# Kernel tuning notes

Hardware: AMD Instinct MI355X
Metric: run time of the kernel (lower is better)

Reference implementation:

```python
import jax, jax.numpy as jnp
import numpy as np

B, S, D_MODEL, FILTER, K, MAX_FRAMES = 16, 512, 512, 512, 3, 2048


def _conv1d(x, w, b):
    # x: [B, C, L], w: [O, I, K], padding=1 -> same length
    y = jax.lax.conv_general_dilated(x, w, window_strides=(1,), padding=[(1, 1)],
                                     dimension_numbers=("NCH", "OIH", "NCH"))
    return y + b[None, :, None]


def _predictor(x, w1, b1, w2, b2, wl, bl):
    # x: [B, L, d] -> scalar track [B, L]
    h = x.transpose(0, 2, 1)                      # [B, d, L]
    h = jax.nn.relu(_conv1d(h, w1, b1))
    h = jax.nn.relu(_conv1d(h, w2, b2))
    h = h.transpose(0, 2, 1)                      # [B, L, filter]
    return (jnp.einsum("blf,f->bl", h, wl[:, 0]) + bl[0])


def _expand_hidden(H, D, max_T):
    # Length regulator: cumsum + searchsorted gather (vectorized repeat_interleave).
    D = jnp.maximum(D, 0).astype(jnp.int32)
    csum = jnp.cumsum(D, axis=1)                  # [B, S]
    t = jnp.arange(max_T, dtype=jnp.int32)        # [T]
    # idx[b, t] = # of cumsum entries <= t  == source token index for frame t
    idx = jax.vmap(lambda c: jnp.searchsorted(c, t, side="right"))(csum)  # [B, T]
    total = csum[:, -1]                           # [B]
    valid = t[None, :] < jnp.minimum(total, max_T)[:, None]               # [B, T]
    idx_safe = jnp.minimum(idx, S - 1)
    He = jnp.take_along_axis(H, idx_safe[:, :, None], axis=1)             # [B, T, d]
    return jnp.where(valid[:, :, None], He, jnp.zeros((), He.dtype))


def setup_inputs() -> dict:
    key = jax.random.key(0)
    ks = jax.random.split(key, 24)
    def w(k, shape, scale=0.05):
        return jax.random.normal(k, shape, dtype=jnp.float32) * scale
    inp = {
        "H": jax.random.normal(ks[0], (B, S, D_MODEL), dtype=jnp.float32),
        "D_gt": jax.random.randint(ks[1], (B, S), 0, 12, dtype=jnp.int32),
        "P_gt": jax.random.normal(ks[2], (B, MAX_FRAMES), dtype=jnp.float32),
        "E_gt": jax.random.normal(ks[3], (B, MAX_FRAMES), dtype=jnp.float32),
    }
    for i, p in enumerate(["dp", "pp", "ep"]):
        kk = jax.random.split(ks[4 + i], 3)
        inp[p + "_w1"] = w(kk[0], (FILTER, D_MODEL, K))
        inp[p + "_b1"] = jnp.zeros((FILTER,), jnp.float32)
        inp[p + "_w2"] = w(kk[1], (FILTER, FILTER, K))
        inp[p + "_b2"] = jnp.zeros((FILTER,), jnp.float32)
        inp[p + "_wl"] = w(kk[2], (FILTER, 1))
        inp[p + "_bl"] = jnp.zeros((1,), jnp.float32)
    inp["pitch_w"] = w(ks[8], (D_MODEL,))
    inp["pitch_b"] = jnp.zeros((D_MODEL,), jnp.float32)
    inp["energy_w"] = w(ks[9], (D_MODEL,))
    inp["energy_b"] = jnp.zeros((D_MODEL,), jnp.float32)
    return inp


def reference(H, D_gt, P_gt, E_gt,
              dp_w1, dp_b1, dp_w2, dp_b2, dp_wl, dp_bl,
              pp_w1, pp_b1, pp_w2, pp_b2, pp_wl, pp_bl,
              ep_w1, ep_b1, ep_w2, ep_b2, ep_wl, ep_bl,
              pitch_w, pitch_b, energy_w, energy_b):
    # Training path (is_inference=False): D = D_gt, P = P_gt, E = E_gt.
    D_pred = _predictor(H, dp_w1, dp_b1, dp_w2, dp_b2, dp_wl, dp_bl)     # [B, S]
    H_exp = _expand_hidden(H, D_gt, MAX_FRAMES)                           # [B, T, d]
    P_pred = _predictor(H_exp, pp_w1, pp_b1, pp_w2, pp_b2, pp_wl, pp_bl)  # [B, T]
    E_pred = _predictor(H_exp, ep_w1, ep_b1, ep_w2, ep_b2, ep_wl, ep_bl)  # [B, T]
    P_proj = P_gt[:, :, None] * pitch_w[None, None, :] + pitch_b          # Linear(1,d)
    E_proj = E_gt[:, :, None] * energy_w[None, None, :] + energy_b
    H_adapted = H_exp + P_proj + E_proj
    return (H_adapted, D_pred, P_pred, E_pred)
```

## Files before the change

kernel.cpp:

```cpp
#include <hip/hip_runtime.h>

#define B_ 16
#define S_ 512
#define C_ 512
#define T_ 2048

typedef __attribute__((ext_vector_type(8))) short short8;
typedef __attribute__((ext_vector_type(4))) float floatx4;

__device__ __forceinline__ unsigned short f2bf(float x) {
    union { float f; unsigned u; } c; c.f = x;
    unsigned r = (c.u + 0x7fffu + ((c.u >> 16) & 1u)) >> 16;
    return (unsigned short)r;
}

__device__ __forceinline__ void gld_lds16(void* l, const void* g) {
    __builtin_amdgcn_global_load_lds(
        (const __attribute__((address_space(1))) void*)g,
        (__attribute__((address_space(3))) void*)l, 16, 0, 0);
}

__global__ void prep_kernel(const float* __restrict__ w0, const float* __restrict__ w1,
                            const float* __restrict__ w2, const float* __restrict__ w3,
                            const float* __restrict__ w4, const float* __restrict__ w5,
                            unsigned short* __restrict__ wpack,
                            const float* __restrict__ H, unsigned short* __restrict__ Hbf,
                            unsigned short* __restrict__ zrow) {
    int blk = blockIdx.x;
    if (blk < 6144) {
        int which = blk >> 10;
        const float* w = which == 0 ? w0 : which == 1 ? w1 : which == 2 ? w2
                       : which == 3 ? w3 : which == 4 ? w4 : w5;
        unsigned short* wp = wpack + (long)which * 786432;
        int i = (blk & 1023) * 256 + threadIdx.x;
        const float* s = w + (long)i * 3;
        wp[i]          = f2bf(s[0]);
        wp[i + 262144] = f2bf(s[1]);
        wp[i + 524288] = f2bf(s[2]);
    } else if (blk < 10240) {
        int i = (blk - 6144) * 256 + threadIdx.x;
        float4 v = *(const float4*)(H + (long)i * 4);
        ushort4 o;
        o.x = f2bf(v.x); o.y = f2bf(v.y); o.z = f2bf(v.z); o.w = f2bf(v.w);
        *(ushort4*)(Hbf + (long)i * 4) = o;
    } else {
        zrow[(blk - 10240) * 256 + threadIdx.x] = 0;
    }
}

__global__ void expand_rowidx_kernel(const int* __restrict__ Dgt, int* __restrict__ ridx) {
    __shared__ int cs[S_];
    int b = blockIdx.x, s = threadIdx.x;
    int d = Dgt[b * S_ + s];
    cs[s] = d < 0 ? 0 : d;
    __syncthreads();
    for (int off = 1; off < S_; off <<= 1) {
        int v = (s >= off) ? cs[s - off] : 0;
        __syncthreads();
        cs[s] += v;
        __syncthreads();
    }
    int total = cs[S_ - 1];
    int limit = total < T_ ? total : T_;
    for (int t = s; t < T_; t += S_) {
        int lo = 0, hi = S_;
        while (lo < hi) { int mid = (lo + hi) >> 1; if (cs[mid] <= t) lo = mid + 1; else hi = mid; }
        if (lo > S_ - 1) lo = S_ - 1;
        ridx[b * T_ + t] = (t < limit) ? lo : -1;
    }
}

__global__ void fill3_kernel(float* __restrict__ D, float* __restrict__ P, float* __restrict__ E,
                             const float* __restrict__ dbl, const float* __restrict__ pbl,
                             const float* __restrict__ ebl) {
    int i = blockIdx.x * 256 + threadIdx.x;
    if (i < 8192) D[i] = dbl[0];
    else if (i < 40960) P[i - 8192] = pbl[0];
    else E[i - 40960] = ebl[0];
}

__global__ void adapt_kernel(const float* __restrict__ H, const int* __restrict__ ridx,
                             const float* __restrict__ Pgt, const float* __restrict__ Egt,
                             const float* __restrict__ pw, const float* __restrict__ pb,
                             const float* __restrict__ ew, const float* __restrict__ eb,
                             float* __restrict__ out) {
    int i = blockIdx.x * 256 + threadIdx.x;
    int f4 = i & 127;
    int p  = i >> 7;
    int b  = p >> 11;
    int r  = ridx[p];
    float pg = Pgt[p], eg = Egt[p];
    int f = f4 << 2;
    float4 pwv = *(const float4*)(pw + f);
    float4 pbv = *(const float4*)(pb + f);
    float4 ewv = *(const float4*)(ew + f);
    float4 ebv = *(const float4*)(eb + f);
    float4 h = make_float4(0.f, 0.f, 0.f, 0.f);
    if (r >= 0) h = *(const float4*)(H + ((long)b * S_ + r) * C_ + f);
    float4 o;
    o.x = h.x + pg * pwv.x + pbv.x + eg * ewv.x + ebv.x;
    o.y = h.y + pg * pwv.y + pbv.y + eg * ewv.y + ebv.y;
    o.z = h.z + pg * pwv.z + pbv.z + eg * ewv.z + ebv.z;
    o.w = h.w + pg * pwv.w + pbv.w + eg * ewv.w + ebv.w;
    *(float4*)(out + (long)p * C_ + f) = o;
}

struct ConvJob {
    const unsigned short* X;
    const int* ridx;
    int Lshift;
    int Bshift;
    const unsigned short* wp;
    const float* bias;
    const float* wl;
    void* dst;
    int nx;
};

__global__ __launch_bounds__(256, 4) void conv_mfma_kernel(
    ConvJob j0, ConvJob j1, const unsigned short* __restrict__ zrow, int mode)
{
    __shared__ unsigned short Wt[3 * 128 * 32];
    __shared__ unsigned short Xt[136 * 32];
    const ConvJob j = (blockIdx.y < 4) ? j0 : j1;
    if ((int)blockIdx.x >= j.nx) return;
    const int tid = threadIdx.x;
    const int m0 = (blockIdx.y & 3) * 128;
    const int n0 = blockIdx.x * 128;
    const int L = 1 << j.Lshift;
    const int b = n0 >> j.Lshift;
    const int t0 = n0 & (L - 1);

    floatx4 acc[4][4];
#pragma unroll
    for (int i = 0; i < 4; ++i)
#pragma unroll
        for (int jj = 0; jj < 4; ++jj) acc[i][jj] = (floatx4){0.f, 0.f, 0.f, 0.f};

    const unsigned short* wptr[6];
#pragma unroll
    for (int q = 0; q < 6; ++q) {
        int idx = tid + q * 256;
        int tap = idx >> 9, rem = idx & 511;
        int row = rem >> 2;
        int sw = (rem & 3) ^ ((row >> 1) & 3);
        wptr[q] = j.wp + (long)tap * (C_ * C_) + (long)(m0 + row) * C_ + sw * 8;
    }
    auto xrow = [&](int rho) -> const unsigned short* {
        int t = t0 - 1 + rho;
        if (t < 0 || t >= L) return zrow;
        int r = j.ridx ? j.ridx[(b << j.Lshift) + t] : t;
        if (r < 0) return zrow;
        return j.X + ((long)(b << j.Bshift) + r) * C_;
    };
    const int xs = tid & 3;
    const int rho0 = tid >> 2, rho1 = 64 + (tid >> 2), rho2 = 128 + (tid >> 2);
    const unsigned short* xptr0 = xrow(rho0) + (xs ^ ((rho0 >> 1) & 3)) * 8;
    const unsigned short* xptr1 = xrow(rho1) + (xs ^ ((rho1 >> 1) & 3)) * 8;
    const unsigned short* xptr2 = (tid < 8) ? (xrow(rho2) + (xs ^ ((rho2 >> 1) & 3)) * 8) : zrow;

    char* wbase = (char*)Wt + (tid >> 6) * 1024;
    char* xbase = (char*)Xt + (tid >> 6) * 1024;

    const int lane = tid & 63;
    const int q = lane >> 4, lr = lane & 15;
    const int wm = (tid >> 6) & 1, wn = tid >> 7;
    const int qsW = (q ^ ((lr >> 1) & 3)) * 8;
    int qsX[3];
#pragma unroll
    for (int tap = 0; tap < 3; ++tap)
        qsX[tap] = (q ^ (((lr + tap) >> 1) & 3)) * 8;

    for (int c0 = 0; c0 < C_; c0 += 32) {
        __syncthreads();
#pragma unroll
        for (int qq = 0; qq < 6; ++qq)
            gld_lds16(wbase + qq * 4096, wptr[qq] + c0);
        gld_lds16(xbase, xptr0 + c0);
        gld_lds16(xbase + 4096, xptr1 + c0);
        if (tid < 8)
            gld_lds16((char*)Xt + 8192, xptr2 + c0);
        __syncthreads();
#pragma unroll
        for (int tap = 0; tap < 3; ++tap) {
            const unsigned short* Wl = Wt + ((tap * 128) + wm * 64 + lr) * 32 + qsW;
            const unsigned short* Xl = Xt + (wn * 64 + lr + tap) * 32 + qsX[tap];
            short8 a[4], bf[4];
#pragma unroll
            for (int i = 0; i < 4; ++i) {
                a[i]  = *(const short8*)(Wl + i * 16 * 32);
                bf[i] = *(const short8*)(Xl + i * 16 * 32);
            }
#pragma unroll
            for (int i = 0; i < 4; ++i)
#pragma unroll
                for (int jj = 0; jj < 4; ++jj)
                    acc[i][jj] = __builtin_amdgcn_mfma_f32_16x16x32_bf16(
                        a[i], bf[jj], acc[i][jj], 0, 0, 0);
        }
    }

    const int fbase = m0 + wm * 64 + q * 4;
    const int pbase = n0 + wn * 64 + lr;
    if (mode == 0) {
        unsigned short* dst = (unsigned short*)j.dst;
#pragma unroll
        for (int i = 0; i < 4; ++i) {
            int f = fbase + i * 16;
            float4 bv = *(const float4*)(j.bias + f);
#pragma unroll
            for (int jj = 0; jj < 4; ++jj) {
                int p = pbase + jj * 16;
                ushort4 o;
                o.x = f2bf(fmaxf(acc[i][jj][0] + bv.x, 0.f));
                o.y = f2bf(fmaxf(acc[i][jj][1] + bv.y, 0.f));
                o.z = f2bf(fmaxf(acc[i][jj][2] + bv.z, 0.f));
                o.w = f2bf(fmaxf(acc[i][jj][3] + bv.w, 0.f));
                *(ushort4*)(dst + (long)p * C_ + f) = o;
            }
        }
    } else {
        float* dst = (float*)j.dst;
#pragma unroll
        for (int jj = 0; jj < 4; ++jj) {
            float s = 0.f;
#pragma unroll
            for (int i = 0; i < 4; ++i) {
                int f = fbase + i * 16;
                float4 bv = *(const float4*)(j.bias + f);
                float4 wv = *(const float4*)(j.wl + f);
                s += fmaxf(acc[i][jj][0] + bv.x, 0.f) * wv.x;
                s += fmaxf(acc[i][jj][1] + bv.y, 0.f) * wv.y;
                s += fmaxf(acc[i][jj][2] + bv.z, 0.f) * wv.z;
                s += fmaxf(acc[i][jj][3] + bv.w, 0.f) * wv.w;
            }
            s += __shfl_xor(s, 16, 64);
            s += __shfl_xor(s, 32, 64);
            if (lane < 16) atomicAdd(dst + pbase + jj * 16, s);
        }
    }
}

extern "C" void kernel_launch(void* const* d_in, const int* in_sizes, int n_in,
                              void* d_out, int out_size, void* d_ws, size_t ws_size,
                              hipStream_t stream) {
    const float* H    = (const float*)d_in[0];
    const int*   Dgt  = (const int*)d_in[1];
    const float* Pgt  = (const float*)d_in[2];
    const float* Egt  = (const float*)d_in[3];
    const float* dp_w1 = (const float*)d_in[4];
    const float* dp_b1 = (const float*)d_in[5];
    const float* dp_w2 = (const float*)d_in[6];
    const float* dp_b2 = (const float*)d_in[7];
    const float* dp_wl = (const float*)d_in[8];
    const float* dp_bl = (const float*)d_in[9];
    const float* pp_w1 = (const float*)d_in[10];
    const float* pp_b1 = (const float*)d_in[11];
    const float* pp_w2 = (const float*)d_in[12];
    const float* pp_b2 = (const float*)d_in[13];
    const float* pp_wl = (const float*)d_in[14];
    const float* pp_bl = (const float*)d_in[15];
    const float* ep_w1 = (const float*)d_in[16];
    const float* ep_b1 = (const float*)d_in[17];
    const float* ep_w2 = (const float*)d_in[18];
    const float* ep_b2 = (const float*)d_in[19];
    const float* ep_wl = (const float*)d_in[20];
    const float* ep_bl = (const float*)d_in[21];
    const float* pitch_w  = (const float*)d_in[22];
    const float* pitch_b  = (const float*)d_in[23];
    const float* energy_w = (const float*)d_in[24];
    const float* energy_b = (const float*)d_in[25];

    float* out     = (float*)d_out;
    float* H_adapt = out;
    float* D_pred  = out + 16777216;
    float* P_pred  = out + 16785408;
    float* E_pred  = out + 16818176;

    char* ws = (char*)d_ws;
    size_t off = 0;
    unsigned short* wpack = (unsigned short*)(ws + off); off += 6UL * 786432UL * 2UL;
    unsigned short* Hbf   = (unsigned short*)(ws + off); off += 4194304UL * 2UL;
    unsigned short* h1a   = (unsigned short*)(ws + off); off += 16777216UL * 2UL;
    unsigned short* h1dp  = (unsigned short*)(ws + off); off += 4194304UL * 2UL;
    unsigned short* zrow  = (unsigned short*)(ws + off); off += 512UL * 2UL;
    off = (off + 255) & ~(size_t)255;
    int* ridx_exp = (int*)(ws + off); off += (size_t)B_ * T_ * 4;

    hipLaunchKernelGGL(prep_kernel, dim3(10242), dim3(256), 0, stream,
                       dp_w1, dp_w2, pp_w1, pp_w2, ep_w1, ep_w2, wpack, H, Hbf, zrow);
    hipLaunchKernelGGL(expand_rowidx_kernel, dim3(B_), dim3(S_), 0, stream, Dgt, ridx_exp);
    hipLaunchKernelGGL(adapt_kernel, dim3(16384), dim3(256), 0, stream,
                       H, ridx_exp, Pgt, Egt, pitch_w, pitch_b, energy_w, energy_b, H_adapt);
    hipLaunchKernelGGL(fill3_kernel, dim3(288), dim3(256), 0, stream,
                       D_pred, P_pred, E_pred, dp_bl, pp_bl, ep_bl);

    ConvJob j_pp1 = { Hbf, ridx_exp, 11, 9, wpack + 2UL * 786432, pp_b1, nullptr, h1a,  256 };
    ConvJob j_dp1 = { Hbf, nullptr,   9, 9, wpack + 0UL * 786432, dp_b1, nullptr, h1dp,  64 };
    ConvJob j_pp2 = { h1a, nullptr,  11, 11, wpack + 3UL * 786432, pp_b2, pp_wl, P_pred, 256 };
    ConvJob j_dp2 = { h1dp, nullptr,  9,  9, wpack + 1UL * 786432, dp_b2, dp_wl, D_pred,  64 };
    ConvJob j_ep1 = { Hbf, ridx_exp, 11, 9, wpack + 4UL * 786432, ep_b1, nullptr, h1a,  256 };
    ConvJob j_ep2 = { h1a, nullptr,  11, 11, wpack + 5UL * 786432, ep_b2, ep_wl, E_pred, 256 };

    hipLaunchKernelGGL(conv_mfma_kernel, dim3(256, 8), dim3(256), 0, stream, j_pp1, j_dp1, zrow, 0);
    hipLaunchKernelGGL(conv_mfma_kernel, dim3(256, 8), dim3(256), 0, stream, j_pp2, j_dp2, zrow, 1);
    hipLaunchKernelGGL(conv_mfma_kernel, dim3(256, 4), dim3(256), 0, stream, j_ep1, j_ep1, zrow, 0);
    hipLaunchKernelGGL(conv_mfma_kernel, dim3(256, 4), dim3(256), 0, stream, j_ep2, j_ep2, zrow, 1);
}
```

Before: 387.9 us.

## Fuse prep kernels and co-schedule pitch/energy/duration convs with adapt in mega kernel

Folds the row-index scan and bias fill into the prep kernel, and merges the adapt gather into the first conv launch as extra blocks. With a second hidden buffer, the pitch, energy and duration conv layers run together in two launches instead of four. The goal is fewer launches, less tail idling and better overlap of the bandwidth-bound adapt pass with MFMA conv work. The cost is an extra 32MB workspace buffer; the new path is gated on the workspace size, with a fallback otherwise.

```diff
diff --git a/kernel.cpp b/kernel.cpp
--- a/kernel.cpp
+++ b/kernel.cpp
@@ -25,84 +25,64 @@
                             const float* __restrict__ w4, const float* __restrict__ w5,
                             unsigned short* __restrict__ wpack,
                             const float* __restrict__ H, unsigned short* __restrict__ Hbf,
-                            unsigned short* __restrict__ zrow) {
+                            unsigned short* __restrict__ zrow,
+                            const int* __restrict__ Dgt, int* __restrict__ ridx,
+                            float* __restrict__ Dp, float* __restrict__ Pp, float* __restrict__ Ep,
+                            const float* __restrict__ dbl, const float* __restrict__ pbl,
+                            const float* __restrict__ ebl) {
+    __shared__ int cs[S_];
+    __shared__ int ps[256];
     int blk = blockIdx.x;
+    int tid = threadIdx.x;
     if (blk < 6144) {
         int which = blk >> 10;
         const float* w = which == 0 ? w0 : which == 1 ? w1 : which == 2 ? w2
                        : which == 3 ? w3 : which == 4 ? w4 : w5;
         unsigned short* wp = wpack + (long)which * 786432;
-        int i = (blk & 1023) * 256 + threadIdx.x;
+        int i = (blk & 1023) * 256 + tid;
         const float* s = w + (long)i * 3;
         wp[i]          = f2bf(s[0]);
         wp[i + 262144] = f2bf(s[1]);
         wp[i + 524288] = f2bf(s[2]);
     } else if (blk < 10240) {
-        int i = (blk - 6144) * 256 + threadIdx.x;
+        int i = (blk - 6144) * 256 + tid;
         float4 v = *(const float4*)(H + (long)i * 4);
         ushort4 o;
         o.x = f2bf(v.x); o.y = f2bf(v.y); o.z = f2bf(v.z); o.w = f2bf(v.w);
         *(ushort4*)(Hbf + (long)i * 4) = o;
+    } else if (blk < 10242) {
+        zrow[(blk - 10240) * 256 + tid] = 0;
+    } else if (blk < 10258) {
+        int b = blk - 10242;
+        int t2 = tid * 2;
+        int d0 = Dgt[b * S_ + t2], d1 = Dgt[b * S_ + t2 + 1];
+        int a0 = d0 < 0 ? 0 : d0, a1 = d1 < 0 ? 0 : d1;
+        ps[tid] = a0 + a1;
+        __syncthreads();
+        for (int off = 1; off < 256; off <<= 1) {
+            int v = (tid >= off) ? ps[tid - off] : 0;
+            __syncthreads();
+            ps[tid] += v;
+            __syncthreads();
+        }
+        int incl = ps[tid];
+        cs[t2] = incl - a1;
+        cs[t2 + 1] = incl;
+        __syncthreads();
+        int total = cs[S_ - 1];
+        int limit = total < T_ ? total : T_;
+        for (int t = tid; t < T_; t += 256) {
+            int lo = 0, hi = S_;
+            while (lo < hi) { int mid = (lo + hi) >> 1; if (cs[mid] <= t) lo = mid + 1; else hi = mid; }
+            if (lo > S_ - 1) lo = S_ - 1;
+            ridx[b * T_ + t] = (t < limit) ? lo : -1;
+        }
     } else {
-        zrow[(blk - 10240) * 256 + threadIdx.x] = 0;
-    }
-}
-
-__global__ void expand_rowidx_kernel(const int* __restrict__ Dgt, int* __restrict__ ridx) {
-    __shared__ int cs[S_];
-    int b = blockIdx.x, s = threadIdx.x;
-    int d = Dgt[b * S_ + s];
-    cs[s] = d < 0 ? 0 : d;
-    __syncthreads();
-    for (int off = 1; off < S_; off <<= 1) {
-        int v = (s >= off) ? cs[s - off] : 0;
-        __syncthreads();
-        cs[s] += v;
-        __syncthreads();
-    }
-    int total = cs[S_ - 1];
-    int limit = total < T_ ? total : T_;
-    for (int t = s; t < T_; t += S_) {
-        int lo = 0, hi = S_;
-        while (lo < hi) { int mid = (lo + hi) >> 1; if (cs[mid] <= t) lo = mid + 1; else hi = mid; }
-        if (lo > S_ - 1) lo = S_ - 1;
-        ridx[b * T_ + t] = (t < limit) ? lo : -1;
-    }
-}
-
-__global__ void fill3_kernel(float* __restrict__ D, float* __restrict__ P, float* __restrict__ E,
-                             const float* __restrict__ dbl, const float* __restrict__ pbl,
-                             const float* __restrict__ ebl) {
-    int i = blockIdx.x * 256 + threadIdx.x;
-    if (i < 8192) D[i] = dbl[0];
-    else if (i < 40960) P[i - 8192] = pbl[0];
-    else E[i - 40960] = ebl[0];
-}
-
-__global__ void adapt_kernel(const float* __restrict__ H, const int* __restrict__ ridx,
-                             const float* __restrict__ Pgt, const float* __restrict__ Egt,
-                             const float* __restrict__ pw, const float* __restrict__ pb,
-                             const float* __restrict__ ew, const float* __restrict__ eb,
-                             float* __restrict__ out) {
-    int i = blockIdx.x * 256 + threadIdx.x;
-    int f4 = i & 127;
-    int p  = i >> 7;
-    int b  = p >> 11;
-    int r  = ridx[p];
-    float pg = Pgt[p], eg = Egt[p];
-    int f = f4 << 2;
-    float4 pwv = *(const float4*)(pw + f);
-    float4 pbv = *(const float4*)(pb + f);
-    float4 ewv = *(const float4*)(ew + f);
-    float4 ebv = *(const float4*)(eb + f);
-    float4 h = make_float4(0.f, 0.f, 0.f, 0.f);
-    if (r >= 0) h = *(const float4*)(H + ((long)b * S_ + r) * C_ + f);
-    float4 o;
-    o.x = h.x + pg * pwv.x + pbv.x + eg * ewv.x + ebv.x;
-    o.y = h.y + pg * pwv.y + pbv.y + eg * ewv.y + ebv.y;
-    o.z = h.z + pg * pwv.z + pbv.z + eg * ewv.z + ebv.z;
-    o.w = h.w + pg * pwv.w + pbv.w + eg * ewv.w + ebv.w;
-    *(float4*)(out + (long)p * C_ + f) = o;
+        int i = (blk - 10258) * 256 + tid;
+        if (i < 8192) Dp[i] = dbl[0];
+        else if (i < 40960) Pp[i - 8192] = pbl[0];
+        else Ep[i - 40960] = ebl[0];
+    }
 }
 
 struct ConvJob {
@@ -114,19 +94,57 @@
     const float* bias;
     const float* wl;
     void* dst;
-    int nx;
+    int nxshift;
 };
 
-__global__ __launch_bounds__(256, 4) void conv_mfma_kernel(
-    ConvJob j0, ConvJob j1, const unsigned short* __restrict__ zrow, int mode)
+__global__ __launch_bounds__(256, 4) void mega_kernel(
+    ConvJob j0, ConvJob j1, ConvJob j2, int e0, int e1, int e2, int mode,
+    const unsigned short* __restrict__ zrow,
+    const float* __restrict__ H, const int* __restrict__ aridx,
+    const float* __restrict__ Pgt, const float* __restrict__ Egt,
+    const float* __restrict__ pw, const float* __restrict__ pb,
+    const float* __restrict__ ew, const float* __restrict__ eb,
+    float* __restrict__ aout)
 {
     __shared__ unsigned short Wt[3 * 128 * 32];
     __shared__ unsigned short Xt[136 * 32];
-    const ConvJob j = (blockIdx.y < 4) ? j0 : j1;
-    if ((int)blockIdx.x >= j.nx) return;
+    const int bx = blockIdx.x;
     const int tid = threadIdx.x;
-    const int m0 = (blockIdx.y & 3) * 128;
-    const int n0 = blockIdx.x * 128;
+
+    if (bx >= e2) {
+        int ab = bx - e2;
+#pragma unroll
+        for (int it = 0; it < 8; ++it) {
+            int i = ab * 256 + tid + it * 524288;
+            int f4 = i & 127;
+            int p  = i >> 7;
+            int b  = p >> 11;
+            int r  = aridx[p];
+            float pg = Pgt[p], eg = Egt[p];
+            int f = f4 << 2;
+            float4 pwv = *(const float4*)(pw + f);
+            float4 pbv = *(const float4*)(pb + f);
+            float4 ewv = *(const float4*)(ew + f);
+            float4 ebv = *(const float4*)(eb + f);
+            float4 h = make_float4(0.f, 0.f, 0.f, 0.f);
+            if (r >= 0) h = *(const float4*)(H + ((long)b * S_ + r) * C_ + f);
+            float4 o;
+            o.x = h.x + pg * pwv.x + pbv.x + eg * ewv.x + ebv.x;
+            o.y = h.y + pg * pwv.y + pbv.y + eg * ewv.y + ebv.y;
+            o.z = h.z + pg * pwv.z + pbv.z + eg * ewv.z + ebv.z;
+            o.w = h.w + pg * pwv.w + pbv.w + eg * ewv.w + ebv.w;
+            *(float4*)(aout + (long)p * C_ + f) = o;
+        }
+        return;
+    }
+
+    ConvJob j;
+    int local;
+    if (bx < e0)      { j = j0; local = bx; }
+    else if (bx < e1) { j = j1; local = bx - e0; }
+    else              { j = j2; local = bx - e1; }
+    const int m0 = (local >> j.nxshift) * 128;
+    const int n0 = (local & ((1 << j.nxshift) - 1)) * 128;
     const int L = 1 << j.Lshift;
     const int b = n0 >> j.Lshift;
     const int t0 = n0 & (L - 1);
@@ -277,33 +295,50 @@
     float* P_pred  = out + 16785408;
     float* E_pred  = out + 16818176;
 
+    const bool par = ws_size >= 94000000ull;
+
     char* ws = (char*)d_ws;
     size_t off = 0;
     unsigned short* wpack = (unsigned short*)(ws + off); off += 6UL * 786432UL * 2UL;
     unsigned short* Hbf   = (unsigned short*)(ws + off); off += 4194304UL * 2UL;
     unsigned short* h1a   = (unsigned short*)(ws + off); off += 16777216UL * 2UL;
+    unsigned short* h1b   = par ? (unsigned short*)(ws + off) : h1a;
+    if (par) off += 16777216UL * 2UL;
     unsigned short* h1dp  = (unsigned short*)(ws + off); off += 4194304UL * 2UL;
     unsigned short* zrow  = (unsigned short*)(ws + off); off += 512UL * 2UL;
     off = (off + 255) & ~(size_t)255;
     int* ridx_exp = (int*)(ws + off); off += (size_t)B_ * T_ * 4;
 
-    hipLaunchKernelGGL(prep_kernel, dim3(10242), dim3(256), 0, stream,
-                       dp_w1, dp_w2, pp_w1, pp_w2, ep_w1, ep_w2, wpack, H, Hbf, zrow);
-    hipLaunchKernelGGL(expand_rowidx_kernel, dim3(B_), dim3(S_), 0, stream, Dgt, ridx_exp);
-    hipLaunchKernelGGL(adapt_kernel, dim3(16384), dim3(256), 0, stream,
-                       H, ridx_exp, Pgt, Egt, pitch_w, pitch_b, energy_w, energy_b, H_adapt);
-    hipLaunchKernelGGL(fill3_kernel, dim3(288), dim3(256), 0, stream,
-                       D_pred, P_pred, E_pred, dp_bl, pp_bl, ep_bl);
-
-    ConvJob j_pp1 = { Hbf, ridx_exp, 11, 9, wpack + 2UL * 786432, pp_b1, nullptr, h1a,  256 };
-    ConvJob j_dp1 = { Hbf, nullptr,   9, 9, wpack + 0UL * 786432, dp_b1, nullptr, h1dp,  64 };
-    ConvJob j_pp2 = { h1a, nullptr,  11, 11, wpack + 3UL * 786432, pp_b2, pp_wl, P_pred, 256 };
-    ConvJob j_dp2 = { h1dp, nullptr,  9,  9, wpack + 1UL * 786432, dp_b2, dp_wl, D_pred,  64 };
-    ConvJob j_ep1 = { Hbf, ridx_exp, 11, 9, wpack + 4UL * 786432, ep_b1, nullptr, h1a,  256 };
-    ConvJob j_ep2 = { h1a, nullptr,  11, 11, wpack + 5UL * 786432, ep_b2, ep_wl, E_pred, 256 };
-
-    hipLaunchKernelGGL(conv_mfma_kernel, dim3(256, 8), dim3(256), 0, stream, j_pp1, j_dp1, zrow, 0);
-    hipLaunchKernelGGL(conv_mfma_kernel, dim3(256, 8), dim3(256), 0, stream, j_pp2, j_dp2, zrow, 1);
-    hipLaunchKernelGGL(conv_mfma_kernel, dim3(256, 4), dim3(256), 0, stream, j_ep1, j_ep1, zrow, 0);
-    hipLaunchKernelGGL(conv_mfma_kernel, dim3(256, 4), dim3(256), 0, stream, j_ep2, j_ep2, zrow, 1);
-}
+    hipLaunchKernelGGL(prep_kernel, dim3(10546), dim3(256), 0, stream,
+                       dp_w1, dp_w2, pp_w1, pp_w2, ep_w1, ep_w2, wpack, H, Hbf, zrow,
+                       Dgt, ridx_exp, D_pred, P_pred, E_pred, dp_bl, pp_bl, ep_bl);
+
+    ConvJob j_pp1 = { Hbf,  ridx_exp, 11,  9, wpack + 2UL * 786432, pp_b1, nullptr, h1a,    8 };
+    ConvJob j_ep1 = { Hbf,  ridx_exp, 11,  9, wpack + 4UL * 786432, ep_b1, nullptr, h1b,    8 };
+    ConvJob j_dp1 = { Hbf,  nullptr,   9,  9, wpack + 0UL * 786432, dp_b1, nullptr, h1dp,   6 };
+    ConvJob j_pp2 = { h1a,  nullptr,  11, 11, wpack + 3UL * 786432, pp_b2, pp_wl,  P_pred, 8 };
+    ConvJob j_ep2 = { h1b,  nullptr,  11, 11, wpack + 5UL * 786432, ep_b2, ep_wl,  E_pred, 8 };
+    ConvJob j_dp2 = { h1dp, nullptr,   9,  9, wpack + 1UL * 786432, dp_b2, dp_wl,  D_pred, 6 };
+
+    if (par) {
+        hipLaunchKernelGGL(mega_kernel, dim3(2304 + 2048), dim3(256), 0, stream,
+                           j_pp1, j_ep1, j_dp1, 1024, 2048, 2304, 0, zrow,
+                           H, ridx_exp, Pgt, Egt, pitch_w, pitch_b, energy_w, energy_b, H_adapt);
+        hipLaunchKernelGGL(mega_kernel, dim3(2304), dim3(256), 0, stream,
+                           j_pp2, j_ep2, j_dp2, 1024, 2048, 2304, 1, zrow,
+                           H, ridx_exp, Pgt, Egt, pitch_w, pitch_b, energy_w, energy_b, H_adapt);
+    } else {
+        hipLaunchKernelGGL(mega_kernel, dim3(1280 + 2048), dim3(256), 0, stream,
+                           j_pp1, j_dp1, j_dp1, 1024, 1280, 1280, 0, zrow,
+                           H, ridx_exp, Pgt, Egt, pitch_w, pitch_b, energy_w, energy_b, H_adapt);
+        hipLaunchKernelGGL(mega_kernel, dim3(1280), dim3(256), 0, stream,
+                           j_pp2, j_dp2, j_dp2, 1024, 1280, 1280, 1, zrow,
+                           H, ridx_exp, Pgt, Egt, pitch_w, pitch_b, energy_w, energy_b, H_adapt);
+        hipLaunchKernelGGL(mega_kernel, dim3(1024), dim3(256), 0, stream,
+                           j_ep1, j_ep1, j_ep1, 1024, 1024, 1024, 0, zrow,
+                           H, ridx_exp, Pgt, Egt, pitch_w, pitch_b, energy_w, energy_b, H_adapt);
+        hipLaunchKernelGGL(mega_kernel, dim3(1024), dim3(256), 0, stream,
+                           j_ep2, j_ep2, j_ep2, 1024, 1024, 1024, 1, zrow,
+                           H, ridx_exp, Pgt, Egt, pitch_w, pitch_b, energy_w, energy_b, H_adapt);
+    }
+}
```

After: 357.5 us. 1.09x faster.
